# Kernel optimization log

Measured on AMD Instinct MI355X. Metric: run time of the kernel, lower is better.

## Reference

```python
import jax, jax.numpy as jnp
import numpy as np

LN_EPS = 1e-5  # torch LayerNorm default


def setup_inputs() -> dict:
    key = jax.random.key(0)
    ks = jax.random.split(key, 8)
    R, B, E, H, NREL = 100, 32, 15000, 16, 237
    return {
        "all_h": jax.random.randint(ks[0], (B,), 0, E, dtype=jnp.int64),
        "all_r": jnp.zeros((B,), dtype=jnp.int64),  # all queries share one relation (asserted in torch code)
        "rule_count": jax.random.randint(ks[1], (R, B, E), 0, 2, dtype=jnp.int32),  # grounding counts (sparse 0/1)
        "rule_emb": jax.random.normal(ks[2], (R, H), dtype=jnp.float32),
        "relation_emb": jax.random.normal(ks[3], (NREL, H), dtype=jnp.float32),
        "ln_g": jnp.ones((H,), dtype=jnp.float32),
        "ln_b": jnp.zeros((H,), dtype=jnp.float32),
        "W1": jax.random.normal(ks[4], (2 * H, 128), dtype=jnp.float32) * 0.1,
        "b1": jnp.zeros((128,), dtype=jnp.float32),
        "W2": jax.random.normal(ks[5], (128, 1), dtype=jnp.float32) * 0.1,
        "b2": jnp.zeros((1,), dtype=jnp.float32),
        "bias": jnp.zeros((E,), dtype=jnp.float32),
    }


def reference(all_h, all_r, rule_count, rule_emb, relation_emb, ln_g, ln_b, W1, b1, W2, b2, bias):
    # rule_count: [R, B, E] grounding counts; candidates are positions with any nonzero count.
    rc = rule_count.astype(jnp.float32)
    cand = rc.sum(0) > 0  # [B, E] candidate mask

    # FuncToNodeSum: weighted sum of rule embeddings per (batch, entity), then LayerNorm + ReLU.
    wvf = jnp.einsum('rbe,rh->beh', rc, rule_emb)  # [B, E, H]
    mu = wvf.mean(-1, keepdims=True)
    var = ((wvf - mu) ** 2).mean(-1, keepdims=True)
    vv = jax.nn.relu((wvf - mu) * jax.lax.rsqrt(var + LN_EPS) * ln_g + ln_b)

    # Concatenate query-relation embedding and score with MLP(2H -> 128 -> 1).
    rel = relation_emb[all_r[0]]  # [H]
    feat = jnp.concatenate([vv, jnp.broadcast_to(rel, vv.shape)], axis=-1)  # [B, E, 2H]
    h = jax.nn.relu(jnp.einsum('beh,hk->bek', feat, W1) + b1)
    out = (jnp.einsum('bek,ko->beo', h, W2) + b2)[..., 0]  # [B, E]

    # Scatter to candidates only (zeros elsewhere), then add entity bias (entity_feature='bias').
    score = jnp.where(cand, out, 0.0) + bias[None, :]
    return score
```

## Files before the change

kernel.cpp:

```cpp
#include <hip/hip_runtime.h>

#define NRULE 100
#define NB    32
#define NE    15000
#define NTOT  (NB * NE)
#define HD    16
#define KMID  128
#define LN_EPS 1e-5f
#define RCHUNK 10

__global__ void precompute_c_kernel(const long long* __restrict__ all_r,
                                    const float* __restrict__ relemb,
                                    const float* __restrict__ W1,
                                    const float* __restrict__ b1,
                                    float* __restrict__ cvec)
{
    const int k = threadIdx.x;
    if (k >= KMID) return;
    const int r = (int)all_r[0];
    float t = b1[k];
#pragma unroll
    for (int h = 0; h < HD; ++h)
        t = fmaf(relemb[r * HD + h], W1[(HD + h) * KMID + k], t);
    cvec[k] = t;
}

__global__ __launch_bounds__(256) void predictor_main_kernel(
    const int*   __restrict__ rc,
    const float* __restrict__ remb,
    const float* __restrict__ ln_g,
    const float* __restrict__ ln_b,
    const float* __restrict__ W1,
    const float* __restrict__ W2,
    const float* __restrict__ b2,
    const float* __restrict__ bias,
    const float* __restrict__ cvec,
    float* __restrict__ out)
{
    const int tid = blockIdx.x * blockDim.x + threadIdx.x;
    if (tid >= NTOT) return;

    float acc[HD];
#pragma unroll
    for (int h = 0; h < HD; ++h) acc[h] = 0.f;
    float ws = 0.f;

    const int* rcp = rc + tid;
#pragma unroll 2
    for (int r0 = 0; r0 < NRULE; r0 += RCHUNK) {
        int v[RCHUNK];
#pragma unroll
        for (int i = 0; i < RCHUNK; ++i)
            v[i] = rcp[(r0 + i) * NTOT];
#pragma unroll
        for (int i = 0; i < RCHUNK; ++i) {
            const float f = (float)v[i];
            ws += f;
#pragma unroll
            for (int h = 0; h < HD; ++h)
                acc[h] = fmaf(f, remb[(r0 + i) * HD + h], acc[h]);
        }
    }

    {
        float mu = 0.f;
#pragma unroll
        for (int h = 0; h < HD; ++h) mu += acc[h];
        mu *= (1.f / HD);
        float var = 0.f;
#pragma unroll
        for (int h = 0; h < HD; ++h) {
            const float d = acc[h] - mu;
            var = fmaf(d, d, var);
        }
        var *= (1.f / HD);
        const float ri = rsqrtf(var + LN_EPS);
#pragma unroll
        for (int h = 0; h < HD; ++h)
            acc[h] = fmaxf(fmaf((acc[h] - mu) * ri, ln_g[h], ln_b[h]), 0.f);
    }

    float o = b2[0];
#pragma unroll 1
    for (int kc = 0; kc < KMID; kc += 8) {
        float t[8];
#pragma unroll
        for (int kk = 0; kk < 8; ++kk) t[kk] = cvec[kc + kk];
#pragma unroll
        for (int h = 0; h < HD; ++h) {
            const float a = acc[h];
#pragma unroll
            for (int kk = 0; kk < 8; ++kk)
                t[kk] = fmaf(a, W1[h * KMID + kc + kk], t[kk]);
        }
#pragma unroll
        for (int kk = 0; kk < 8; ++kk)
            o = fmaf(fmaxf(t[kk], 0.f), W2[kc + kk], o);
    }

    o = (ws > 0.f) ? o : 0.f;
    out[tid] = o + bias[tid % NE];
}

extern "C" void kernel_launch(void* const* d_in, const int* in_sizes, int n_in,
                              void* d_out, int out_size, void* d_ws, size_t ws_size,
                              hipStream_t stream)
{
    const long long* all_r = (const long long*)d_in[1];
    const int*   rc     = (const int*)d_in[2];
    const float* remb   = (const float*)d_in[3];
    const float* relemb = (const float*)d_in[4];
    const float* ln_g   = (const float*)d_in[5];
    const float* ln_b   = (const float*)d_in[6];
    const float* W1     = (const float*)d_in[7];
    const float* b1     = (const float*)d_in[8];
    const float* W2     = (const float*)d_in[9];
    const float* b2     = (const float*)d_in[10];
    const float* bias   = (const float*)d_in[11];
    float* out  = (float*)d_out;
    float* cvec = (float*)d_ws;

    hipLaunchKernelGGL(precompute_c_kernel, dim3(1), dim3(128), 0, stream,
                       all_r, relemb, W1, b1, cvec);

    const int blocks = (NTOT + 255) / 256;
    hipLaunchKernelGGL(predictor_main_kernel, dim3(blocks), dim3(256), 0, stream,
                       rc, remb, ln_g, ln_b, W1, W2, b2, bias, cvec, out);
}
```

Before: 74.83 us.

## Process two entities per thread with packed float2 FMA and int2 loads

Each thread now handles two adjacent (batch, entity) positions. It loads rule counts as int2 and uses v2f packed FMA, which can map to packed FP32 instructions, for the rule accumulation, the LayerNorm and the MLP. The candidate mask switches from a float sum to an integer OR, and the output is stored as a float2. The aim is fewer memory transactions per element and better ALU throughput, at the cost of half as many threads and more registers, which may reduce occupancy and latency hiding for a memory-bound load of 192MB.

New measurement: 62.52 us. 16.4% less time.

```diff
diff --git a/kernel.cpp b/kernel.cpp
--- a/kernel.cpp
+++ b/kernel.cpp
@@ -8,6 +8,8 @@
 #define KMID  128
 #define LN_EPS 1e-5f
 #define RCHUNK 10
+
+typedef float v2f __attribute__((ext_vector_type(2)));
 
 __global__ void precompute_c_kernel(const long long* __restrict__ all_r,
                                     const float* __restrict__ relemb,
@@ -37,69 +39,102 @@
     const float* __restrict__ cvec,
     float* __restrict__ out)
 {
-    const int tid = blockIdx.x * blockDim.x + threadIdx.x;
-    if (tid >= NTOT) return;
+    const int tid  = blockIdx.x * blockDim.x + threadIdx.x;
+    const int base = tid * 2;
+    if (base >= NTOT) return;
 
-    float acc[HD];
+    v2f acc[2][8];
 #pragma unroll
-    for (int h = 0; h < HD; ++h) acc[h] = 0.f;
-    float ws = 0.f;
+    for (int e = 0; e < 2; ++e)
+#pragma unroll
+        for (int hh = 0; hh < 8; ++hh) acc[e][hh] = (v2f){0.f, 0.f};
+    int c0 = 0, c1 = 0;
 
-    const int* rcp = rc + tid;
+    const int* rcp = rc + base;
 #pragma unroll 2
     for (int r0 = 0; r0 < NRULE; r0 += RCHUNK) {
-        int v[RCHUNK];
+        int2 v[RCHUNK];
 #pragma unroll
         for (int i = 0; i < RCHUNK; ++i)
-            v[i] = rcp[(r0 + i) * NTOT];
+            v[i] = *reinterpret_cast<const int2*>(rcp + (r0 + i) * NTOT);
 #pragma unroll
         for (int i = 0; i < RCHUNK; ++i) {
-            const float f = (float)v[i];
-            ws += f;
+            c0 |= v[i].x; c1 |= v[i].y;
+            const float f0 = (float)v[i].x;
+            const float f1 = (float)v[i].y;
+            const v2f f02 = {f0, f0};
+            const v2f f12 = {f1, f1};
+            const v2f* rb = (const v2f*)(remb + (r0 + i) * HD);
 #pragma unroll
-            for (int h = 0; h < HD; ++h)
-                acc[h] = fmaf(f, remb[(r0 + i) * HD + h], acc[h]);
+            for (int hh = 0; hh < 8; ++hh) {
+                const v2f w = rb[hh];
+                acc[0][hh] = __builtin_elementwise_fma(f02, w, acc[0][hh]);
+                acc[1][hh] = __builtin_elementwise_fma(f12, w, acc[1][hh]);
+            }
         }
     }
 
-    {
-        float mu = 0.f;
+    const float b2v = b2[0];
+    const v2f* g2  = (const v2f*)ln_g;
+    const v2f* bb2 = (const v2f*)ln_b;
+    const v2f* cv2 = (const v2f*)cvec;
+    const v2f* w12 = (const v2f*)W1;
+    const v2f* w22 = (const v2f*)W2;
+    const v2f zero = {0.f, 0.f};
+
+    float o[2];
 #pragma unroll
-        for (int h = 0; h < HD; ++h) mu += acc[h];
-        mu *= (1.f / HD);
-        float var = 0.f;
+    for (int e = 0; e < 2; ++e) {
+        v2f mu2 = zero;
 #pragma unroll
-        for (int h = 0; h < HD; ++h) {
-            const float d = acc[h] - mu;
-            var = fmaf(d, d, var);
+        for (int hh = 0; hh < 8; ++hh) mu2 += acc[e][hh];
+        const float mu = (mu2.x + mu2.y) * (1.f / HD);
+        const v2f mub = {mu, mu};
+        v2f var2 = zero;
+#pragma unroll
+        for (int hh = 0; hh < 8; ++hh) {
+            const v2f d = acc[e][hh] - mub;
+            var2 = __builtin_elementwise_fma(d, d, var2);
         }
-        var *= (1.f / HD);
+        const float var = (var2.x + var2.y) * (1.f / HD);
         const float ri = rsqrtf(var + LN_EPS);
+        const v2f ri2 = {ri, ri};
 #pragma unroll
-        for (int h = 0; h < HD; ++h)
-            acc[h] = fmaxf(fmaf((acc[h] - mu) * ri, ln_g[h], ln_b[h]), 0.f);
+        for (int hh = 0; hh < 8; ++hh) {
+            const v2f t = (acc[e][hh] - mub) * ri2;
+            acc[e][hh] = __builtin_elementwise_max(
+                __builtin_elementwise_fma(t, g2[hh], bb2[hh]), zero);
+        }
+
+        v2f o2 = {b2v, 0.f};
+#pragma unroll 1
+        for (int kc = 0; kc < KMID; kc += 8) {
+            v2f t2[4];
+#pragma unroll
+            for (int kk = 0; kk < 4; ++kk) t2[kk] = cv2[(kc >> 1) + kk];
+#pragma unroll
+            for (int h = 0; h < HD; ++h) {
+                const v2f av = acc[e][h >> 1];
+                const float a = (h & 1) ? av.y : av.x;
+                const v2f a2 = {a, a};
+#pragma unroll
+                for (int kk = 0; kk < 4; ++kk)
+                    t2[kk] = __builtin_elementwise_fma(a2, w12[h * 64 + (kc >> 1) + kk], t2[kk]);
+            }
+#pragma unroll
+            for (int kk = 0; kk < 4; ++kk) {
+                const v2f tr = __builtin_elementwise_max(t2[kk], zero);
+                o2 = __builtin_elementwise_fma(tr, w22[(kc >> 1) + kk], o2);
+            }
+        }
+        o[e] = o2.x + o2.y;
     }
 
-    float o = b2[0];
-#pragma unroll 1
-    for (int kc = 0; kc < KMID; kc += 8) {
-        float t[8];
-#pragma unroll
-        for (int kk = 0; kk < 8; ++kk) t[kk] = cvec[kc + kk];
-#pragma unroll
-        for (int h = 0; h < HD; ++h) {
-            const float a = acc[h];
-#pragma unroll
-            for (int kk = 0; kk < 8; ++kk)
-                t[kk] = fmaf(a, W1[h * KMID + kc + kk], t[kk]);
-        }
-#pragma unroll
-        for (int kk = 0; kk < 8; ++kk)
-            o = fmaf(fmaxf(t[kk], 0.f), W2[kc + kk], o);
-    }
-
-    o = (ws > 0.f) ? o : 0.f;
-    out[tid] = o + bias[tid % NE];
+    const int m = base % NE;
+    float2 res;
+    res.x = ((c0 != 0) ? o[0] : 0.f) + bias[m];
+    res.y = ((c1 != 0) ? o[1] : 0.f) + bias[m + 1];
+    *reinterpret_cast<float2*>(out + base) = res;
 }
 
 extern "C" void kernel_launch(void* const* d_in, const int* in_sizes, int n_in,
@@ -123,7 +158,8 @@
     hipLaunchKernelGGL(precompute_c_kernel, dim3(1), dim3(128), 0, stream,
                        all_r, relemb, W1, b1, cvec);
 
-    const int blocks = (NTOT + 255) / 256;
+    const int threads = NTOT / 2;
+    const int blocks  = (threads + 255) / 256;
     hipLaunchKernelGGL(predictor_main_kernel, dim3(blocks), dim3(256), 0, stream,
                        rc, remb, ln_g, ln_b, W1, W2, b2, bias, cvec, out);
 }
```
